# Kernel optimization log

Hardware: AMD Instinct MI355X
Metric: run time of the kernel (lower is better)

Reference implementation:

```python
import jax, jax.numpy as jnp
import numpy as np

B, H, W, C = 4, 64, 64, 256
C8 = C // 8

def setup_inputs() -> dict:
    key = jax.random.key(0)
    k1, k2, k3, k4 = jax.random.split(key, 4)
    # glorot-uniform-ish init for 1x1 conv kernels stored as [Cin, Cout]
    def glorot(k, cin, cout):
        lim = np.sqrt(6.0 / (cin + cout)).astype(np.float32)
        return jax.random.uniform(k, (cin, cout), jnp.float32, -lim, lim)
    return {
        "x": jax.random.normal(k1, (B, H, W, C), jnp.float32),
        "kernel_f": glorot(k2, C, C8),
        "kernel_g": glorot(k3, C, C8),
        "kernel_h": glorot(k4, C, C),
        "gamma": jnp.zeros((1,), jnp.float32),
    }

def reference(x, kernel_f, kernel_g, kernel_h, gamma):
    b, h, w, c = x.shape
    n = h * w
    xf = x.reshape(b, n, c)                       # [B, N, C]
    # 1x1 convs == per-position matmuls
    f = jnp.einsum('bnc,cd->bnd', xf, kernel_f)   # [B, N, C/8]
    g = jnp.einsum('bnc,cd->bnd', xf, kernel_g)   # [B, N, C/8]
    hh = jnp.einsum('bnc,cd->bnd', xf, kernel_h)  # [B, N, C]
    s = jnp.einsum('bnd,bmd->bnm', g, f)          # [B, N, N]
    beta = jax.nn.softmax(s, axis=-1)
    o = jnp.einsum('bnm,bmc->bnc', beta, hh)      # [B, N, C]
    o = o.reshape(b, h, w, c)
    return gamma * o + x
```

## Files before the change

### kernel.cpp

```cpp
#include <hip/hip_runtime.h>
#include <hip/hip_bf16.h>

typedef __bf16 bf16x8 __attribute__((ext_vector_type(8)));
typedef float f32x4 __attribute__((ext_vector_type(4)));
typedef float f32x16 __attribute__((ext_vector_type(16)));
typedef unsigned short u16;
typedef unsigned int u32;
typedef const __attribute__((address_space(1))) u32 gu32;
typedef __attribute__((address_space(3))) u32 lu32;

__device__ __forceinline__ u16 f2bf_rne(float f){
  union { float f; u32 u; } v; v.f = f;
  u32 r = v.u + 0x7fffu + ((v.u >> 16) & 1u);
  return (u16)(r >> 16);
}
__device__ __forceinline__ u32 pack_trunc(float a, float b){
  union { float f; u32 u; } x, y; x.f = a; y.f = b;
  return (x.u >> 16) | (y.u & 0xffff0000u);
}
__device__ __forceinline__ void stage16(const u16* g, u16* l){
  __builtin_amdgcn_global_load_lds((gu32*)g, (lu32*)l, 16, 0, 0);
}

__global__ __launch_bounds__(256) void prep_kernel(
    const float* __restrict__ Wf, const float* __restrict__ Wg,
    const float* __restrict__ Wh, u16* __restrict__ WcatT){
  __shared__ float tile[32][33];
  const int tx = threadIdx.x & 31, ty = threadIdx.x >> 5;
  const int k0 = blockIdx.x * 32, n0 = blockIdx.y * 32;
  #pragma unroll
  for (int i = 0; i < 4; ++i){
    int k = k0 + ty + i * 8, n = n0 + tx;
    float v;
    if (n < 256)      v = Wh[k * 256 + n];
    else if (n < 288) v = Wf[k * 32 + (n - 256)];
    else              v = Wg[k * 32 + (n - 288)];
    tile[ty + i * 8][tx] = v;
  }
  __syncthreads();
  #pragma unroll
  for (int i = 0; i < 4; ++i){
    int n = n0 + ty + i * 8, k = k0 + tx;
    WcatT[n * 256 + k] = f2bf_rne(tile[tx][ty + i * 8]);
  }
}

__global__ __launch_bounds__(256) void proj_kernel(
    const float* __restrict__ x, const u16* __restrict__ WcatT,
    u16* __restrict__ Qg, u16* __restrict__ Kg, u16* __restrict__ Vfrag)
{
  __shared__ __align__(16) u16 smem[256 * 72];
  u16 (*xb)[264] = (u16(*)[264])smem;
  u16 (*Vr)[72]  = (u16(*)[72])smem;

  const int tid = threadIdx.x;
  const int lane = tid & 63, wave = tid >> 6;
  const int L = lane & 15, quad = lane >> 4;
  const int n0 = blockIdx.x * 64;

  const float4* xsrc = (const float4*)(x + (size_t)n0 * 256);
  #pragma unroll
  for (int j = 0; j < 16; ++j){
    int idx = j * 256 + tid;
    int row = idx >> 6, col4 = idx & 63;
    float4 v = xsrc[idx];
    u32 p0 = (u32)f2bf_rne(v.x) | ((u32)f2bf_rne(v.y) << 16);
    u32 p1 = (u32)f2bf_rne(v.z) | ((u32)f2bf_rne(v.w) << 16);
    *(uint2*)&xb[row][col4 * 4] = make_uint2(p0, p1);
  }
  __syncthreads();

  f32x4 acc[20];
  #pragma unroll
  for (int cc = 0; cc < 20; ++cc) acc[cc] = (f32x4){0.f, 0.f, 0.f, 0.f};

  #pragma unroll
  for (int kk = 0; kk < 8; ++kk){
    bf16x8 a = *(const bf16x8*)&xb[wave * 16 + L][kk * 32 + quad * 8];
    #pragma unroll
    for (int cc = 0; cc < 20; ++cc){
      bf16x8 bfr = *(const bf16x8*)(WcatT + (size_t)(cc * 16 + L) * 256 + kk * 32 + quad * 8);
      acc[cc] = __builtin_amdgcn_mfma_f32_16x16x32_bf16(a, bfr, acc[cc], 0, 0, 0);
    }
  }

  #pragma unroll
  for (int cc = 16; cc < 20; ++cc){
    u16* dst = (cc < 18) ? Kg : Qg;
    int c = (cc & 1) * 16 + L;
    #pragma unroll
    for (int r = 0; r < 4; ++r){
      int row = n0 + wave * 16 + quad * 4 + r;
      dst[(size_t)row * 32 + c] = f2bf_rne(acc[cc][r]);
    }
  }

  __syncthreads();

  #pragma unroll
  for (int cc = 0; cc < 16; ++cc){
    int c = cc * 16 + L;
    #pragma unroll
    for (int r = 0; r < 4; ++r){
      int tn = wave * 16 + quad * 4 + r;
      int p  = ((tn & 15) << 2) | (tn >> 4);
      Vr[c][p] = f2bf_rne(acc[cc][r]);
    }
  }
  __syncthreads();

  u16* Vblk = Vfrag + (size_t)blockIdx.x * (256 * 64);
  #pragma unroll
  for (int i = 0; i < 8; ++i){
    *(uint4*)(Vblk + (size_t)(i * 256 + tid) * 8) = *(const uint4*)&Vr[tid][i * 8];
  }
}

__global__ __launch_bounds__(512, 4) void flash_kernel(
    const u16* __restrict__ Qg, const u16* __restrict__ Kg, const u16* __restrict__ Vfrag,
    u16* __restrict__ Opart, float* __restrict__ Lpart)
{
  constexpr float LOG2E = 1.44269504088896340736f;
  constexpr float SH    = -92.33248261689366f;
  __shared__ __align__(16) u16 Plds[128][72];
  __shared__ __align__(16) u16 Vlds[16384];

  const int tid = threadIdx.x, lane = tid & 63, wave = tid >> 6;
  const int L = lane & 15, quad = lane >> 4;
  const int m32 = lane & 31, h32 = lane >> 5;
  const int b = blockIdx.y, split = blockIdx.z;
  const int qblk = blockIdx.x * 128;
  const int qquad = wave & 3, chalf = wave >> 2;

  const u16* Qb = Qg + (size_t)(b * 4096) * 32;
  const u16* Kb = Kg + (size_t)(b * 4096) * 32;
  const u16* Vb = Vfrag + (size_t)b * (64 * 256 * 64);

  int g = split * 16;
  {
    const u16* vt = Vb + (size_t)g * (256 * 64);
    #pragma unroll
    for (int i = 0; i < 4; ++i){
      int chunk = wave * 4 + i;
      stage16(vt + chunk * 512 + lane * 8, &Vlds[chunk * 512]);
    }
  }
  bf16x8 qa = *(const bf16x8*)(Qb + (size_t)(qblk + wave * 16 + L) * 32 + quad * 8);
  const u16* kp0 = Kb + (size_t)(g * 64 + L) * 32 + quad * 8;
  bf16x8 kc0 = *(const bf16x8*)(kp0);
  bf16x8 kc1 = *(const bf16x8*)(kp0 + 512);
  bf16x8 kc2 = *(const bf16x8*)(kp0 + 1024);
  bf16x8 kc3 = *(const bf16x8*)(kp0 + 1536);

  bf16x8 vones;
  #pragma unroll
  for (int i = 0; i < 8; ++i) vones[i] = (__bf16)1.0f;

  f32x16 acc[4];
  #pragma unroll
  for (int ct = 0; ct < 4; ++ct)
    #pragma unroll
    for (int i = 0; i < 16; ++i) acc[ct][i] = 0.f;
  f32x4 accl = (f32x4){0.f, 0.f, 0.f, 0.f};
  const f32x4 zero = (f32x4){0.f, 0.f, 0.f, 0.f};

  for (int kt = 0; kt < 16; ++kt){
    f32x4 s0 = __builtin_amdgcn_mfma_f32_16x16x32_bf16(qa, kc0, zero, 0, 0, 0);
    f32x4 s1 = __builtin_amdgcn_mfma_f32_16x16x32_bf16(qa, kc1, zero, 0, 0, 0);
    f32x4 s2 = __builtin_amdgcn_mfma_f32_16x16x32_bf16(qa, kc2, zero, 0, 0, 0);
    f32x4 s3 = __builtin_amdgcn_mfma_f32_16x16x32_bf16(qa, kc3, zero, 0, 0, 0);

    #pragma unroll
    for (int r = 0; r < 4; ++r){
      float p0 = exp2f(fmaf(s0[r], LOG2E, SH));
      float p1 = exp2f(fmaf(s1[r], LOG2E, SH));
      float p2 = exp2f(fmaf(s2[r], LOG2E, SH));
      float p3 = exp2f(fmaf(s3[r], LOG2E, SH));
      *(uint2*)&Plds[wave * 16 + quad * 4 + r][L * 4] =
          make_uint2(pack_trunc(p0, p1), pack_trunc(p2, p3));
    }
    bf16x8 pa0 = *(const bf16x8*)&Plds[wave * 16 + L][quad * 8];
    bf16x8 pa1 = *(const bf16x8*)&Plds[wave * 16 + L][32 + quad * 8];
    accl = __builtin_amdgcn_mfma_f32_16x16x32_bf16(pa0, vones, accl, 0, 0, 0);
    accl = __builtin_amdgcn_mfma_f32_16x16x32_bf16(pa1, vones, accl, 0, 0, 0);

    __syncthreads();

    bf16x8 kn0, kn1, kn2, kn3;
    if (kt < 15){
      const u16* kpn = Kb + (size_t)((g + 1) * 64 + L) * 32 + quad * 8;
      kn0 = *(const bf16x8*)(kpn);
      kn1 = *(const bf16x8*)(kpn + 512);
      kn2 = *(const bf16x8*)(kpn + 1024);
      kn3 = *(const bf16x8*)(kpn + 1536);
    }

    #pragma unroll
    for (int ks = 0; ks < 4; ++ks){
      bf16x8 af = *(const bf16x8*)&Plds[qquad * 32 + m32][ks * 16 + h32 * 8];
      const int vbase = ((ks * 2 + h32) * 256 + chalf * 128 + m32) * 8;
      #pragma unroll
      for (int ct = 0; ct < 4; ++ct){
        bf16x8 vf = *(const bf16x8*)&Vlds[vbase + ct * 32 * 8];
        acc[ct] = __builtin_amdgcn_mfma_f32_32x32x16_bf16(af, vf, acc[ct], 0, 0, 0);
      }
    }

    __syncthreads();

    if (kt < 15){
      const u16* vt = Vb + (size_t)(g + 1) * (256 * 64);
      #pragma unroll
      for (int i = 0; i < 4; ++i){
        int chunk = wave * 4 + i;
        stage16(vt + chunk * 512 + lane * 8, &Vlds[chunk * 512]);
      }
      kc0 = kn0; kc1 = kn1; kc2 = kn2; kc3 = kn3;
    }
    ++g;
  }

  u16* Ob = Opart + ((size_t)split * 16384 + (size_t)b * 4096 + qblk) * 256;
  #pragma unroll
  for (int ct = 0; ct < 4; ++ct){
    #pragma unroll
    for (int rg = 0; rg < 16; ++rg){
      int row = qquad * 32 + (rg & 3) + 8 * (rg >> 2) + 4 * h32;
      int c = chalf * 128 + ct * 32 + m32;
      Ob[(size_t)row * 256 + c] = (u16)(__float_as_uint(acc[ct][rg]) >> 16);
    }
  }
  if (L == 0){
    float* Lp = Lpart + split * 16384 + b * 4096 + qblk + wave * 16;
    #pragma unroll
    for (int r = 0; r < 4; ++r) Lp[quad * 4 + r] = accl[r];
  }
}

__global__ __launch_bounds__(256) void combine_kernel(
    const float* __restrict__ x, const float* __restrict__ gamma,
    const u16* __restrict__ Opart, const float* __restrict__ Lpart,
    float* __restrict__ out)
{
  const int t = threadIdx.x;
  const int row = blockIdx.x * 4 + (t >> 6);
  const int c0 = (t & 63) * 4;
  const size_t base = (size_t)row * 256 + c0;
  float os0 = 0.f, os1 = 0.f, os2 = 0.f, os3 = 0.f, ls = 0.f;
  #pragma unroll
  for (int s = 0; s < 4; ++s){
    ls += Lpart[s * 16384 + row];
    uint2 u = *(const uint2*)(Opart + (size_t)s * 16384 * 256 + base);
    os0 += __uint_as_float(u.x << 16);
    os1 += __uint_as_float(u.x & 0xffff0000u);
    os2 += __uint_as_float(u.y << 16);
    os3 += __uint_as_float(u.y & 0xffff0000u);
  }
  const float r = gamma[0] / ls;
  float4 xv = *(const float4*)(x + base);
  float4 o;
  o.x = os0 * r + xv.x;
  o.y = os1 * r + xv.y;
  o.z = os2 * r + xv.z;
  o.w = os3 * r + xv.w;
  *(float4*)(out + base) = o;
}

extern "C" void kernel_launch(void* const* d_in, const int* in_sizes, int n_in,
                              void* d_out, int out_size, void* d_ws, size_t ws_size,
                              hipStream_t stream) {
  const float* x     = (const float*)d_in[0];
  const float* Wf    = (const float*)d_in[1];
  const float* Wg    = (const float*)d_in[2];
  const float* Wh    = (const float*)d_in[3];
  const float* gamma = (const float*)d_in[4];
  float* out = (float*)d_out;

  u16* p = (u16*)d_ws;
  u16* Qg    = p;  p += 16384 * 32;
  u16* Kg    = p;  p += 16384 * 32;
  u16* Vfrag = p;  p += 4 * 64 * 256 * 64;
  u16* WcatT = p;  p += 320 * 256;
  u16* Opart = p;  p += (size_t)4 * 16384 * 256;
  float* Lpart = (float*)p;

  prep_kernel<<<dim3(8, 10), 256, 0, stream>>>(Wf, Wg, Wh, WcatT);
  proj_kernel<<<256, 256, 0, stream>>>(x, WcatT, Qg, Kg, Vfrag);
  flash_kernel<<<dim3(32, 4, 4), 512, 0, stream>>>(Qg, Kg, Vfrag, Opart, Lpart);
  combine_kernel<<<4096, 256, 0, stream>>>(x, gamma, Opart, Lpart, out);
}
```

Measured before the change: 159.6 us.

## Split attention over channel halves, double-buffer V, widen projection and combine blocks

The flash kernel's grid now splits the 256 output channels across two blocks, so each block computes half the PV product. Each block stages half of V into a double-buffered LDS tile that is prefetched one step ahead, and the barriers are lighter waits on lgkmcnt only. The row sum is now accumulated in registers from the fp32 probabilities and reduced with shuffles, replacing the MFMA against a ones vector. Elsewhere, the projection kernel uses 512 threads with column halves split across waves, and the combine kernel processes 8 channels per thread. The cost is that QK^T and the exponentials are computed twice, once per channel half, and the row sum now comes from unrounded fp32 values rather than the truncated bf16 ones used in PV.

```diff
diff --git a/kernel.cpp b/kernel.cpp
--- a/kernel.cpp
+++ b/kernel.cpp
@@ -21,6 +21,7 @@
 __device__ __forceinline__ void stage16(const u16* g, u16* l){
   __builtin_amdgcn_global_load_lds((gu32*)g, (lu32*)l, 16, 0, 0);
 }
+#define BARRIER_LGKM() asm volatile("s_waitcnt lgkmcnt(0)\n\ts_barrier" ::: "memory")
 
 __global__ __launch_bounds__(256) void prep_kernel(
     const float* __restrict__ Wf, const float* __restrict__ Wg,
@@ -45,7 +46,7 @@
   }
 }
 
-__global__ __launch_bounds__(256) void proj_kernel(
+__global__ __launch_bounds__(512) void proj_kernel(
     const float* __restrict__ x, const u16* __restrict__ WcatT,
     u16* __restrict__ Qg, u16* __restrict__ Kg, u16* __restrict__ Vfrag)
 {
@@ -56,12 +57,13 @@
   const int tid = threadIdx.x;
   const int lane = tid & 63, wave = tid >> 6;
   const int L = lane & 15, quad = lane >> 4;
+  const int rowgrp = wave >> 1, colhalf = wave & 1;
   const int n0 = blockIdx.x * 64;
 
   const float4* xsrc = (const float4*)(x + (size_t)n0 * 256);
   #pragma unroll
-  for (int j = 0; j < 16; ++j){
-    int idx = j * 256 + tid;
+  for (int j = 0; j < 8; ++j){
+    int idx = j * 512 + tid;
     int row = idx >> 6, col4 = idx & 63;
     float4 v = xsrc[idx];
     u32 p0 = (u32)f2bf_rne(v.x) | ((u32)f2bf_rne(v.y) << 16);
@@ -70,49 +72,57 @@
   }
   __syncthreads();
 
-  f32x4 acc[20];
-  #pragma unroll
-  for (int cc = 0; cc < 20; ++cc) acc[cc] = (f32x4){0.f, 0.f, 0.f, 0.f};
+  f32x4 acc[10];
+  #pragma unroll
+  for (int cc = 0; cc < 10; ++cc) acc[cc] = (f32x4){0.f, 0.f, 0.f, 0.f};
 
   #pragma unroll
   for (int kk = 0; kk < 8; ++kk){
-    bf16x8 a = *(const bf16x8*)&xb[wave * 16 + L][kk * 32 + quad * 8];
-    #pragma unroll
-    for (int cc = 0; cc < 20; ++cc){
-      bf16x8 bfr = *(const bf16x8*)(WcatT + (size_t)(cc * 16 + L) * 256 + kk * 32 + quad * 8);
+    bf16x8 a = *(const bf16x8*)&xb[rowgrp * 16 + L][kk * 32 + quad * 8];
+    #pragma unroll
+    for (int cc = 0; cc < 10; ++cc){
+      int ccg = colhalf * 10 + cc;
+      bf16x8 bfr = *(const bf16x8*)(WcatT + (size_t)(ccg * 16 + L) * 256 + kk * 32 + quad * 8);
       acc[cc] = __builtin_amdgcn_mfma_f32_16x16x32_bf16(a, bfr, acc[cc], 0, 0, 0);
     }
   }
 
-  #pragma unroll
-  for (int cc = 16; cc < 20; ++cc){
-    u16* dst = (cc < 18) ? Kg : Qg;
-    int c = (cc & 1) * 16 + L;
-    #pragma unroll
-    for (int r = 0; r < 4; ++r){
-      int row = n0 + wave * 16 + quad * 4 + r;
-      dst[(size_t)row * 32 + c] = f2bf_rne(acc[cc][r]);
+  if (colhalf){
+    #pragma unroll
+    for (int cc = 6; cc < 10; ++cc){
+      int ccg = 10 + cc;
+      u16* dst = (ccg < 18) ? Kg : Qg;
+      int c = (ccg & 1) * 16 + L;
+      #pragma unroll
+      for (int r = 0; r < 4; ++r){
+        int row = n0 + rowgrp * 16 + quad * 4 + r;
+        dst[(size_t)row * 32 + c] = f2bf_rne(acc[cc][r]);
+      }
     }
   }
 
   __syncthreads();
 
-  #pragma unroll
-  for (int cc = 0; cc < 16; ++cc){
-    int c = cc * 16 + L;
-    #pragma unroll
-    for (int r = 0; r < 4; ++r){
-      int tn = wave * 16 + quad * 4 + r;
-      int p  = ((tn & 15) << 2) | (tn >> 4);
-      Vr[c][p] = f2bf_rne(acc[cc][r]);
+  {
+    const int cmax = colhalf ? 6 : 10;
+    for (int cc = 0; cc < cmax; ++cc){
+      int ccg = colhalf * 10 + cc;
+      int c = ccg * 16 + L;
+      #pragma unroll
+      for (int r = 0; r < 4; ++r){
+        int tn = rowgrp * 16 + quad * 4 + r;
+        int p  = ((tn & 15) << 2) | (tn >> 4);
+        Vr[c][p] = f2bf_rne(acc[cc][r]);
+      }
     }
   }
   __syncthreads();
 
   u16* Vblk = Vfrag + (size_t)blockIdx.x * (256 * 64);
   #pragma unroll
-  for (int i = 0; i < 8; ++i){
-    *(uint4*)(Vblk + (size_t)(i * 256 + tid) * 8) = *(const uint4*)&Vr[tid][i * 8];
+  for (int i = 0; i < 4; ++i){
+    int idx = i * 512 + tid;
+    *(uint4*)(Vblk + (size_t)idx * 8) = *(const uint4*)&Vr[idx & 255][(idx >> 8) * 8];
   }
 }
 
@@ -123,48 +133,67 @@
   constexpr float LOG2E = 1.44269504088896340736f;
   constexpr float SH    = -92.33248261689366f;
   __shared__ __align__(16) u16 Plds[128][72];
-  __shared__ __align__(16) u16 Vlds[16384];
+  __shared__ __align__(16) u16 Vlds[2][8192];
 
   const int tid = threadIdx.x, lane = tid & 63, wave = tid >> 6;
   const int L = lane & 15, quad = lane >> 4;
   const int m32 = lane & 31, h32 = lane >> 5;
-  const int b = blockIdx.y, split = blockIdx.z;
+  const int qquad = wave >> 1, chalf2 = wave & 1;
+  const int b = blockIdx.y >> 1, chalf = blockIdx.y & 1;
+  const int split = blockIdx.z;
   const int qblk = blockIdx.x * 128;
-  const int qquad = wave & 3, chalf = wave >> 2;
 
   const u16* Qb = Qg + (size_t)(b * 4096) * 32;
   const u16* Kb = Kg + (size_t)(b * 4096) * 32;
   const u16* Vb = Vfrag + (size_t)b * (64 * 256 * 64);
 
-  int g = split * 16;
+  const int g0 = split * 16;
+
   {
-    const u16* vt = Vb + (size_t)g * (256 * 64);
-    #pragma unroll
-    for (int i = 0; i < 4; ++i){
-      int chunk = wave * 4 + i;
-      stage16(vt + chunk * 512 + lane * 8, &Vlds[chunk * 512]);
+    const u16* vt = Vb + (size_t)g0 * (256 * 64);
+    #pragma unroll
+    for (int i = 0; i < 2; ++i){
+      int c = wave * 2 + i;
+      int ph = c >> 1, c64 = c & 1;
+      stage16(vt + (size_t)(ph * 256 + chalf * 128 + c64 * 64) * 8 + lane * 8,
+              &Vlds[0][(ph * 128 + c64 * 64) * 8]);
     }
   }
   bf16x8 qa = *(const bf16x8*)(Qb + (size_t)(qblk + wave * 16 + L) * 32 + quad * 8);
-  const u16* kp0 = Kb + (size_t)(g * 64 + L) * 32 + quad * 8;
+  const u16* kp0 = Kb + (size_t)(g0 * 64 + L) * 32 + quad * 8;
   bf16x8 kc0 = *(const bf16x8*)(kp0);
   bf16x8 kc1 = *(const bf16x8*)(kp0 + 512);
   bf16x8 kc2 = *(const bf16x8*)(kp0 + 1024);
   bf16x8 kc3 = *(const bf16x8*)(kp0 + 1536);
 
-  bf16x8 vones;
-  #pragma unroll
-  for (int i = 0; i < 8; ++i) vones[i] = (__bf16)1.0f;
-
-  f32x16 acc[4];
-  #pragma unroll
-  for (int ct = 0; ct < 4; ++ct)
+  f32x16 acc[2];
+  #pragma unroll
+  for (int ct = 0; ct < 2; ++ct)
     #pragma unroll
     for (int i = 0; i < 16; ++i) acc[ct][i] = 0.f;
-  f32x4 accl = (f32x4){0.f, 0.f, 0.f, 0.f};
+  float lsum[4] = {0.f, 0.f, 0.f, 0.f};
   const f32x4 zero = (f32x4){0.f, 0.f, 0.f, 0.f};
 
   for (int kt = 0; kt < 16; ++kt){
+    const int g = g0 + kt;
+
+    bf16x8 kn0, kn1, kn2, kn3;
+    if (kt < 15){
+      const u16* vt = Vb + (size_t)(g + 1) * (256 * 64);
+      #pragma unroll
+      for (int i = 0; i < 2; ++i){
+        int c = wave * 2 + i;
+        int ph = c >> 1, c64 = c & 1;
+        stage16(vt + (size_t)(ph * 256 + chalf * 128 + c64 * 64) * 8 + lane * 8,
+                &Vlds[(kt + 1) & 1][(ph * 128 + c64 * 64) * 8]);
+      }
+      const u16* kpn = Kb + (size_t)((g + 1) * 64 + L) * 32 + quad * 8;
+      kn0 = *(const bf16x8*)(kpn);
+      kn1 = *(const bf16x8*)(kpn + 512);
+      kn2 = *(const bf16x8*)(kpn + 1024);
+      kn3 = *(const bf16x8*)(kpn + 1536);
+    }
+
     f32x4 s0 = __builtin_amdgcn_mfma_f32_16x16x32_bf16(qa, kc0, zero, 0, 0, 0);
     f32x4 s1 = __builtin_amdgcn_mfma_f32_16x16x32_bf16(qa, kc1, zero, 0, 0, 0);
     f32x4 s2 = __builtin_amdgcn_mfma_f32_16x16x32_bf16(qa, kc2, zero, 0, 0, 0);
@@ -176,64 +205,50 @@
       float p1 = exp2f(fmaf(s1[r], LOG2E, SH));
       float p2 = exp2f(fmaf(s2[r], LOG2E, SH));
       float p3 = exp2f(fmaf(s3[r], LOG2E, SH));
+      lsum[r] += (p0 + p1) + (p2 + p3);
       *(uint2*)&Plds[wave * 16 + quad * 4 + r][L * 4] =
           make_uint2(pack_trunc(p0, p1), pack_trunc(p2, p3));
     }
-    bf16x8 pa0 = *(const bf16x8*)&Plds[wave * 16 + L][quad * 8];
-    bf16x8 pa1 = *(const bf16x8*)&Plds[wave * 16 + L][32 + quad * 8];
-    accl = __builtin_amdgcn_mfma_f32_16x16x32_bf16(pa0, vones, accl, 0, 0, 0);
-    accl = __builtin_amdgcn_mfma_f32_16x16x32_bf16(pa1, vones, accl, 0, 0, 0);
-
-    __syncthreads();
-
-    bf16x8 kn0, kn1, kn2, kn3;
-    if (kt < 15){
-      const u16* kpn = Kb + (size_t)((g + 1) * 64 + L) * 32 + quad * 8;
-      kn0 = *(const bf16x8*)(kpn);
-      kn1 = *(const bf16x8*)(kpn + 512);
-      kn2 = *(const bf16x8*)(kpn + 1024);
-      kn3 = *(const bf16x8*)(kpn + 1536);
-    }
+
+    BARRIER_LGKM();
 
     #pragma unroll
     for (int ks = 0; ks < 4; ++ks){
       bf16x8 af = *(const bf16x8*)&Plds[qquad * 32 + m32][ks * 16 + h32 * 8];
-      const int vbase = ((ks * 2 + h32) * 256 + chalf * 128 + m32) * 8;
+      const int vbase = ((ks * 2 + h32) * 128 + chalf2 * 64 + m32) * 8;
       #pragma unroll
-      for (int ct = 0; ct < 4; ++ct){
-        bf16x8 vf = *(const bf16x8*)&Vlds[vbase + ct * 32 * 8];
+      for (int ct = 0; ct < 2; ++ct){
+        bf16x8 vf = *(const bf16x8*)&Vlds[kt & 1][vbase + ct * 32 * 8];
         acc[ct] = __builtin_amdgcn_mfma_f32_32x32x16_bf16(af, vf, acc[ct], 0, 0, 0);
       }
     }
 
-    __syncthreads();
-
-    if (kt < 15){
-      const u16* vt = Vb + (size_t)(g + 1) * (256 * 64);
-      #pragma unroll
-      for (int i = 0; i < 4; ++i){
-        int chunk = wave * 4 + i;
-        stage16(vt + chunk * 512 + lane * 8, &Vlds[chunk * 512]);
-      }
-      kc0 = kn0; kc1 = kn1; kc2 = kn2; kc3 = kn3;
-    }
-    ++g;
+    BARRIER_LGKM();
+
+    if (kt < 15){ kc0 = kn0; kc1 = kn1; kc2 = kn2; kc3 = kn3; }
   }
 
   u16* Ob = Opart + ((size_t)split * 16384 + (size_t)b * 4096 + qblk) * 256;
   #pragma unroll
-  for (int ct = 0; ct < 4; ++ct){
+  for (int ct = 0; ct < 2; ++ct){
     #pragma unroll
     for (int rg = 0; rg < 16; ++rg){
       int row = qquad * 32 + (rg & 3) + 8 * (rg >> 2) + 4 * h32;
-      int c = chalf * 128 + ct * 32 + m32;
+      int c = chalf * 128 + chalf2 * 64 + ct * 32 + m32;
       Ob[(size_t)row * 256 + c] = (u16)(__float_as_uint(acc[ct][rg]) >> 16);
     }
   }
-  if (L == 0){
+  #pragma unroll
+  for (int r = 0; r < 4; ++r){
+    lsum[r] += __shfl_xor(lsum[r], 1);
+    lsum[r] += __shfl_xor(lsum[r], 2);
+    lsum[r] += __shfl_xor(lsum[r], 4);
+    lsum[r] += __shfl_xor(lsum[r], 8);
+  }
+  if (chalf == 0 && L == 0){
     float* Lp = Lpart + split * 16384 + b * 4096 + qblk + wave * 16;
     #pragma unroll
-    for (int r = 0; r < 4; ++r) Lp[quad * 4 + r] = accl[r];
+    for (int r = 0; r < 4; ++r) Lp[quad * 4 + r] = lsum[r];
   }
 }
 
@@ -243,27 +258,36 @@
     float* __restrict__ out)
 {
   const int t = threadIdx.x;
-  const int row = blockIdx.x * 4 + (t >> 6);
-  const int c0 = (t & 63) * 4;
+  const int row = blockIdx.x * 8 + (t >> 5);
+  const int c0 = (t & 31) * 8;
   const size_t base = (size_t)row * 256 + c0;
-  float os0 = 0.f, os1 = 0.f, os2 = 0.f, os3 = 0.f, ls = 0.f;
+  float os[8];
+  #pragma unroll
+  for (int i = 0; i < 8; ++i) os[i] = 0.f;
+  float ls = 0.f;
   #pragma unroll
   for (int s = 0; s < 4; ++s){
     ls += Lpart[s * 16384 + row];
-    uint2 u = *(const uint2*)(Opart + (size_t)s * 16384 * 256 + base);
-    os0 += __uint_as_float(u.x << 16);
-    os1 += __uint_as_float(u.x & 0xffff0000u);
-    os2 += __uint_as_float(u.y << 16);
-    os3 += __uint_as_float(u.y & 0xffff0000u);
+    uint4 u = *(const uint4*)(Opart + (size_t)s * 16384 * 256 + base);
+    os[0] += __uint_as_float(u.x << 16);
+    os[1] += __uint_as_float(u.x & 0xffff0000u);
+    os[2] += __uint_as_float(u.y << 16);
+    os[3] += __uint_as_float(u.y & 0xffff0000u);
+    os[4] += __uint_as_float(u.z << 16);
+    os[5] += __uint_as_float(u.z & 0xffff0000u);
+    os[6] += __uint_as_float(u.w << 16);
+    os[7] += __uint_as_float(u.w & 0xffff0000u);
   }
   const float r = gamma[0] / ls;
-  float4 xv = *(const float4*)(x + base);
-  float4 o;
-  o.x = os0 * r + xv.x;
-  o.y = os1 * r + xv.y;
-  o.z = os2 * r + xv.z;
-  o.w = os3 * r + xv.w;
-  *(float4*)(out + base) = o;
+  float4 x0 = *(const float4*)(x + base);
+  float4 x1 = *(const float4*)(x + base + 4);
+  float4 o0, o1;
+  o0.x = os[0] * r + x0.x;  o0.y = os[1] * r + x0.y;
+  o0.z = os[2] * r + x0.z;  o0.w = os[3] * r + x0.w;
+  o1.x = os[4] * r + x1.x;  o1.y = os[5] * r + x1.y;
+  o1.z = os[6] * r + x1.z;  o1.w = os[7] * r + x1.w;
+  *(float4*)(out + base)     = o0;
+  *(float4*)(out + base + 4) = o1;
 }
 
 extern "C" void kernel_launch(void* const* d_in, const int* in_sizes, int n_in,
@@ -285,7 +309,7 @@
   float* Lpart = (float*)p;
 
   prep_kernel<<<dim3(8, 10), 256, 0, stream>>>(Wf, Wg, Wh, WcatT);
-  proj_kernel<<<256, 256, 0, stream>>>(x, WcatT, Qg, Kg, Vfrag);
-  flash_kernel<<<dim3(32, 4, 4), 512, 0, stream>>>(Qg, Kg, Vfrag, Opart, Lpart);
-  combine_kernel<<<4096, 256, 0, stream>>>(x, gamma, Opart, Lpart, out);
-}
+  proj_kernel<<<256, 512, 0, stream>>>(x, WcatT, Qg, Kg, Vfrag);
+  flash_kernel<<<dim3(32, 8, 4), 512, 0, stream>>>(Qg, Kg, Vfrag, Opart, Lpart);
+  combine_kernel<<<2048, 256, 0, stream>>>(x, gamma, Opart, Lpart, out);
+}
```

Result: slower. 181.8 us (+13.9%).
